# Performance work log

Hardware: AMD Instinct MI355X
Metric: run time of the kernel (lower is better)

The kernel has to match this reference:

```python
import jax, jax.numpy as jnp
import numpy as np

N = 4096          # batch size / number of points
D_DATA = 1024     # data feature dim
D_LATENT = 64     # latent dim
REG_LAMBDA = 0.5


def _pdist(x):
    """Pairwise Euclidean distance matrix [N, N] via the gram trick.

    Equivalent to norm(x[None, :, :] - x[:, None, :], axis=-1) but avoids the
    N x N x D intermediate. Safe sqrt so the (zero) diagonal has zero gradient.
    """
    sq = jnp.sum(x * x, axis=-1)                      # [N]
    g = x @ x.T                                       # [N, N] gram
    d2 = jnp.maximum(sq[:, None] + sq[None, :] - 2.0 * g, 0.0)
    pos = d2 > 0
    d = jnp.sqrt(jnp.where(pos, d2, 1.0))
    return jnp.where(pos, d, 0.0)


def _mst_edges(dist):
    """Edges (i, j) of the minimum spanning tree of the complete graph with
    edge weights dist[i, j] (0d persistent homology death edges).
    Prim's algorithm, vectorized per step via lax.scan. Returns [N-1, 2] int32.
    """
    n = dist.shape[0]
    in_tree = jnp.zeros(n, dtype=bool).at[0].set(True)
    min_dist = dist[0]                                # best distance to tree
    min_src = jnp.zeros(n, dtype=jnp.int32)           # tree node achieving it

    def step(carry, _):
        in_tree, min_dist, min_src = carry
        masked = jnp.where(in_tree, jnp.inf, min_dist)
        j = jnp.argmin(masked).astype(jnp.int32)
        edge = jnp.stack([min_src[j], j])
        in_tree = in_tree.at[j].set(True)
        dj = dist[j]
        upd = dj < min_dist
        min_dist = jnp.where(upd, dj, min_dist)
        min_src = jnp.where(upd, j, min_src)
        return (in_tree, min_dist, min_src), edge

    _, edges = jax.lax.scan(step, (in_tree, min_dist, min_src), None, length=n - 1)
    return edges  # [N-1, 2]


def _gather(dist, edges):
    return dist[edges[:, 0], edges[:, 1]]  # [N-1]


def setup_inputs() -> dict:
    key = jax.random.key(0)
    k1, k2, k3 = jax.random.split(key, 3)
    return {
        "y_true": jax.random.normal(k1, (N, D_DATA), dtype=jnp.float32),
        "latent": jax.random.normal(k2, (N, D_LATENT), dtype=jnp.float32),
        "y_pred": jax.random.normal(k3, (N, D_DATA), dtype=jnp.float32),
        "latent_norm": jnp.array(1.0, dtype=jnp.float32),
    }


def reference(y_true, latent, y_pred, latent_norm):
    # keras MSE: mean over last axis -> per-sample vector [N]
    ae_loss = jnp.mean((y_true - y_pred) ** 2, axis=-1)

    data_distances = _pdist(y_true)
    data_distances = data_distances / jnp.max(data_distances)
    latent_distances = _pdist(latent) / latent_norm

    e_data = _mst_edges(jax.lax.stop_gradient(data_distances))
    data_loss = jnp.mean((_gather(data_distances, e_data)
                          - _gather(latent_distances, e_data)) ** 2)

    e_lat = _mst_edges(jax.lax.stop_gradient(latent_distances))
    latent_loss = jnp.mean((_gather(data_distances, e_lat)
                            - _gather(latent_distances, e_lat)) ** 2)

    topo_loss = data_loss + latent_loss
    return ae_loss + REG_LAMBDA * topo_loss  # [N] (scalar topo broadcast)
```

## Files before the change

kernel.cpp:

```cpp
#include <hip/hip_runtime.h>
#include <math.h>

#define N_PTS 4096
#define DD 1024
#define DL 64
#define NEDGE (N_PTS - 1)
#define B_ROUNDS 12
#define NT 32

typedef __attribute__((ext_vector_type(8))) short short8;
typedef __attribute__((ext_vector_type(4))) float floatx4;
typedef __attribute__((ext_vector_type(4))) unsigned short ushortx4;

__device__ __forceinline__ unsigned short f2bf(float f) {
  unsigned u = __float_as_uint(f);
  u = u + 0x7FFFu + ((u >> 16) & 1u);
  return (unsigned short)(u >> 16);
}

__global__ __launch_bounds__(256) void ae_sq_kernel(const float* __restrict__ yt,
                                                    const float* __restrict__ yp,
                                                    float* __restrict__ out,
                                                    float* __restrict__ sqD,
                                                    unsigned short* __restrict__ Xb) {
  int row = blockIdx.x, tid = threadIdx.x;
  const float4* a = (const float4*)(yt + (size_t)row * DD);
  const float4* b = (const float4*)(yp + (size_t)row * DD);
  float4 va = a[tid], vb = b[tid];
  ushortx4 o = {f2bf(va.x), f2bf(va.y), f2bf(va.z), f2bf(va.w)};
  *(ushortx4*)(Xb + (size_t)row * DD + tid * 4) = o;
  float e0 = va.x - vb.x, e1 = va.y - vb.y, e2 = va.z - vb.z, e3 = va.w - vb.w;
  float se = e0 * e0 + e1 * e1 + e2 * e2 + e3 * e3;
  float ss = va.x * va.x + va.y * va.y + va.z * va.z + va.w * va.w;
  for (int off = 32; off > 0; off >>= 1) {
    se += __shfl_down(se, off);
    ss += __shfl_down(ss, off);
  }
  __shared__ float sse[4], sss[4];
  int lane = tid & 63, w = tid >> 6;
  if (lane == 0) { sse[w] = se; sss[w] = ss; }
  __syncthreads();
  if (tid == 0) {
    out[row] = (sse[0] + sse[1] + sse[2] + sse[3]) * (1.0f / DD);
    sqD[row] = sss[0] + sss[1] + sss[2] + sss[3];
  }
}

__global__ __launch_bounds__(256) void sql_kernel(const float* __restrict__ lat,
                                                  float* __restrict__ sqL,
                                                  unsigned short* __restrict__ Lb) {
  int row = blockIdx.x * 4 + (threadIdx.x >> 6);
  int lane = threadIdx.x & 63;
  float v = lat[(size_t)row * DL + lane];
  Lb[(size_t)row * DL + lane] = f2bf(v);
  float s = v * v;
  for (int off = 32; off > 0; off >>= 1) s += __shfl_down(s, off);
  if (lane == 0) sqL[row] = s;
}

__global__ __launch_bounds__(256) void boruvka_init(unsigned short* __restrict__ comp,
                                                    unsigned long long* __restrict__ bestKey,
                                                    int* __restrict__ numRoots,
                                                    int* __restrict__ edgeCnt,
                                                    const float* __restrict__ sqD,
                                                    const float* __restrict__ sqL,
                                                    unsigned int* __restrict__ normbits) {
  int i = blockIdx.x * 256 + threadIdx.x;
  if (i < N_PTS) {
    comp[i] = (unsigned short)i;
    comp[N_PTS + i] = (unsigned short)i;
    bestKey[i] = ~0ULL;
    bestKey[N_PTS + i] = ~0ULL;
  }
  if (i == 0) {
    numRoots[0] = N_PTS; numRoots[1] = N_PTS;
    edgeCnt[0] = 0; edgeCnt[1] = 0;
  }
  if (blockIdx.x < 2) {
    const float* s = blockIdx.x ? sqL : sqD;
    int tid = threadIdx.x;
    float m = 0.f;
#pragma unroll
    for (int k = 0; k < 16; ++k) m = fmaxf(m, s[tid + k * 256]);
    for (int off = 32; off > 0; off >>= 1) m = fmaxf(m, __shfl_down(m, off));
    __shared__ float sm[4];
    int lane = tid & 63, w = tid >> 6;
    if (lane == 0) sm[w] = m;
    __syncthreads();
    if (tid == 0)
      normbits[blockIdx.x] = __float_as_uint(fmaxf(fmaxf(sm[0], sm[1]), fmaxf(sm[2], sm[3])));
  }
}

__global__ __launch_bounds__(256) void dist_mfma(const unsigned short* __restrict__ Xb,
                                                 const unsigned short* __restrict__ Lb,
                                                 const float* __restrict__ sqD,
                                                 const float* __restrict__ sqL,
                                                 unsigned short* __restrict__ dD,
                                                 unsigned short* __restrict__ dL,
                                                 const unsigned int* __restrict__ normbits,
                                                 unsigned int* __restrict__ maxbits) {
  int inst = blockIdx.y;
  const unsigned short* X = inst ? Lb : Xb;
  const float* sq = inst ? sqL : sqD;
  unsigned short* dist = inst ? dL : dD;
  int K = inst ? DL : DD;
  float scale = 65535.0f / (2.0f * sqrtf(__uint_as_float(normbits[inst])) + 1e-12f);

  int bi = 0, rem = blockIdx.x, span = NT;
  while (rem >= span) { rem -= span; ++bi; --span; }
  int bj = bi + rem;
  int row0 = bi * 128, col0 = bj * 128;

  __shared__ short As[128 * 40];
  __shared__ short Bs[128 * 40];
  int tid = threadIdx.x;
  int wave = tid >> 6, lane = tid & 63;
  int m = lane & 15, q = lane >> 4;
  int rw = (wave >> 1) * 64, cw = (wave & 1) * 64;

  floatx4 acc[4][4];
#pragma unroll
  for (int mi = 0; mi < 4; ++mi)
#pragma unroll
    for (int ni = 0; ni < 4; ++ni) acc[mi][ni] = {0.f, 0.f, 0.f, 0.f};

  int s0 = tid, s1 = tid + 256;
  int r0 = s0 >> 2, p0 = s0 & 3, r1 = s1 >> 2, p1 = s1 & 3;

  for (int k0 = 0; k0 < K; k0 += 32) {
    short8 a0 = *(const short8*)(X + (size_t)(row0 + r0) * K + k0 + p0 * 8);
    short8 a1 = *(const short8*)(X + (size_t)(row0 + r1) * K + k0 + p1 * 8);
    short8 b0 = *(const short8*)(X + (size_t)(col0 + r0) * K + k0 + p0 * 8);
    short8 b1 = *(const short8*)(X + (size_t)(col0 + r1) * K + k0 + p1 * 8);
    __syncthreads();
    *(short8*)&As[r0 * 40 + p0 * 8] = a0;
    *(short8*)&As[r1 * 40 + p1 * 8] = a1;
    *(short8*)&Bs[r0 * 40 + p0 * 8] = b0;
    *(short8*)&Bs[r1 * 40 + p1 * 8] = b1;
    __syncthreads();
    short8 aF[4], bF[4];
#pragma unroll
    for (int mi = 0; mi < 4; ++mi)
      aF[mi] = *(const short8*)&As[(rw + mi * 16 + m) * 40 + q * 8];
#pragma unroll
    for (int ni = 0; ni < 4; ++ni)
      bF[ni] = *(const short8*)&Bs[(cw + ni * 16 + m) * 40 + q * 8];
#pragma unroll
    for (int mi = 0; mi < 4; ++mi)
#pragma unroll
      for (int ni = 0; ni < 4; ++ni)
        acc[mi][ni] = __builtin_amdgcn_mfma_f32_16x16x32_bf16(aF[mi], bF[ni],
                                                              acc[mi][ni], 0, 0, 0);
  }

  float bmax = 0.f;
#pragma unroll
  for (int mi = 0; mi < 4; ++mi) {
    int i0 = row0 + rw + mi * 16 + q * 4;
    float s_i[4] = {sq[i0], sq[i0 + 1], sq[i0 + 2], sq[i0 + 3]};
#pragma unroll
    for (int ni = 0; ni < 4; ++ni) {
      int j = col0 + cw + ni * 16 + m;
      float sj = sq[j];
      ushortx4 tvec;
#pragma unroll
      for (int r = 0; r < 4; ++r) {
        float d2 = s_i[r] + sj - 2.f * acc[mi][ni][r];
        float d = d2 > 0.f ? sqrtf(d2) : 0.f;
        bmax = fmaxf(bmax, d);
        unsigned short u = (unsigned short)fminf(d * scale, 65535.0f);
        dist[(size_t)(i0 + r) * N_PTS + j] = u;
        tvec[r] = u;
      }
      *(ushortx4*)&dist[(size_t)j * N_PTS + i0] = tvec;
    }
  }
  if (inst == 0) {
    for (int off = 32; off > 0; off >>= 1) bmax = fmaxf(bmax, __shfl_down(bmax, off));
    __shared__ float bm[4];
    if (lane == 0) bm[wave] = bmax;
    __syncthreads();
    if (tid == 0)
      atomicMax(maxbits, __float_as_uint(fmaxf(fmaxf(bm[0], bm[1]), fmaxf(bm[2], bm[3]))));
  }
}

__global__ __launch_bounds__(256) void boruvka_scan0(const unsigned short* __restrict__ dD,
                                                     const unsigned short* __restrict__ dL,
                                                     unsigned int* __restrict__ segKey,
                                                     unsigned long long* __restrict__ bestKey) {
  int inst = blockIdx.y;
  const unsigned short* dist = inst ? dL : dD;
  unsigned int* segK = segKey + (size_t)inst * N_PTS * 64;
  unsigned long long* bkI = bestKey + (size_t)inst * N_PTS;
  int tid = threadIdx.x, wave = tid >> 6, lane = tid & 63;
  int row = blockIdx.x * 4 + wave;
  const uint4* rowp = (const uint4*)(dist + (size_t)row * N_PTS);
  unsigned mk = 0xFFFFFFFFu, fk = 0xFFFFFFFFu;
  int colbase = lane * 64;
#pragma unroll
  for (int t = 0; t < 8; ++t) {
    uint4 v = rowp[lane * 8 + t];
    unsigned e[8] = {v.x & 0xFFFFu, v.x >> 16, v.y & 0xFFFFu, v.y >> 16,
                     v.z & 0xFFFFu, v.z >> 16, v.w & 0xFFFFu, v.w >> 16};
#pragma unroll
    for (int u = 0; u < 8; ++u) {
      int col = colbase + t * 8 + u;
      unsigned key = (e[u] << 12) | (unsigned)col;
      mk = min(mk, key);
      if (col != row) fk = min(fk, key);
    }
  }
  segK[(size_t)row * 64 + lane] = mk;
#pragma unroll
  for (int off = 32; off > 0; off >>= 1) fk = min(fk, __shfl_xor(fk, off));
  if (lane == 0) {
    unsigned dd16 = fk >> 12;
    int j = (int)(fk & 0xFFFu);
    int lo = row < j ? row : j, hi = row < j ? j : row;
    bkI[row] = ((unsigned long long)dd16 << 24) |
               ((unsigned long long)lo << 12) | (unsigned long long)hi;
  }
}

__global__ __launch_bounds__(256) void boruvka_scan(const unsigned short* __restrict__ dD,
                                                    const unsigned short* __restrict__ dL,
                                                    const unsigned int* __restrict__ segKey,
                                                    const unsigned short* __restrict__ comp,
                                                    unsigned long long* __restrict__ bestKey,
                                                    const int* __restrict__ numRoots) {
  int inst = blockIdx.y;
  if (numRoots[inst] <= 1) return;
  const unsigned short* dist = inst ? dL : dD;
  const unsigned int* segK = segKey + (size_t)inst * N_PTS * 64;
  const unsigned short* compI = comp + (size_t)inst * N_PTS;
  unsigned long long* bkI = bestKey + (size_t)inst * N_PTS;
  int tid = threadIdx.x, wave = tid >> 6, lane = tid & 63;

  int row = blockIdx.x * 4 + wave;
  unsigned myc = compI[row];
  unsigned skey = segK[(size_t)row * 64 + lane];
#pragma unroll
  for (int k = 2; k <= 64; k <<= 1)
#pragma unroll
    for (int j = k >> 1; j > 0; j >>= 1) {
      unsigned p = __shfl_xor(skey, j);
      unsigned mn = min(skey, p), mx = max(skey, p);
      skey = (((lane & k) == 0) == ((lane & j) == 0)) ? mn : mx;
    }
  unsigned best = 0xFFFFFFFFu;
  const unsigned short* rowp = dist + (size_t)row * N_PTS;
  int i = 0;
  while (i < 64) {
    unsigned k0 = __shfl(skey, i);
    if (k0 >= best) break;
    unsigned k1 = (i < 63) ? __shfl(skey, i + 1) : 0xFFFFFFFFu;
    int b0 = (int)(k0 & 0xFC0u);
    unsigned d0v = rowp[b0 + lane];
    unsigned c0v = compI[b0 + lane];
    unsigned cand = (c0v != myc) ? ((d0v << 12) | (unsigned)(b0 + lane)) : 0xFFFFFFFFu;
    if (k1 < best) {
      int b1 = (int)(k1 & 0xFC0u);
      unsigned d1v = rowp[b1 + lane];
      unsigned c1v = compI[b1 + lane];
      unsigned c2 = (c1v != myc) ? ((d1v << 12) | (unsigned)(b1 + lane)) : 0xFFFFFFFFu;
      cand = min(cand, c2);
    }
#pragma unroll
    for (int off = 32; off > 0; off >>= 1) cand = min(cand, __shfl_xor(cand, off));
    best = min(best, cand);
    i += 2;
  }
  if (lane == 0 && best != 0xFFFFFFFFu) {
    unsigned dd16 = best >> 12;
    int j = (int)(best & 0xFFFu);
    int lo = row < j ? row : j, hi = row < j ? j : row;
    unsigned long long key40 = ((unsigned long long)dd16 << 24) |
                               ((unsigned long long)lo << 12) | (unsigned long long)hi;
    if (key40 < bkI[myc]) atomicMin(&bkI[myc], key40);
  }
}

__global__ __launch_bounds__(1024) void boruvka_merge(unsigned short* __restrict__ comp,
                                                      unsigned long long* __restrict__ bestKey,
                                                      int* __restrict__ numRoots,
                                                      int2* __restrict__ edges,
                                                      int* __restrict__ edgeCnt) {
  int inst = blockIdx.x;
  if (numRoots[inst] <= 1) return;
  unsigned short* compI = comp + (size_t)inst * N_PTS;
  unsigned long long* bkI = bestKey + (size_t)inst * N_PTS;
  edges += (size_t)inst * NEDGE;

  __shared__ unsigned short comp_s[N_PTS];
  __shared__ unsigned short parent_s[N_PTS];
  __shared__ unsigned long long key_s[N_PTS];
  __shared__ int wtot[16], wbase[16];
  __shared__ int rootCnt, changed;
  int tid = threadIdx.x, lane = tid & 63, w = tid >> 6;
  if (tid == 0) rootCnt = 0;
  for (int i = tid; i < N_PTS / 8; i += 1024)
    ((uint4*)comp_s)[i] = ((const uint4*)compI)[i];
  for (int i = tid; i < N_PTS / 2; i += 1024)
    ((uint4*)key_s)[i] = ((const uint4*)bkI)[i];
  __syncthreads();

  int cnt = 0;
  int2 ebuf[4];
#pragma unroll
  for (int k = 0; k < 4; ++k) {
    int c = tid + k * 1024;
    unsigned short p = (unsigned short)c;
    if (comp_s[c] == c) {
      unsigned long long key = key_s[c];
      bkI[c] = ~0ULL;
      if (key != ~0ULL) {
        int lo = (int)((key >> 12) & 0xFFF), hi = (int)(key & 0xFFF);
        int c2 = (comp_s[lo] == c) ? comp_s[hi] : comp_s[lo];
        bool mutual = (key_s[c2] == key);
        bool add;
        if (mutual) {
          if (c < c2) add = true;
          else { p = (unsigned short)c2; add = false; }
        } else { p = (unsigned short)c2; add = true; }
        if (add) ebuf[cnt++] = make_int2(lo, hi);
      }
    }
    parent_s[c] = p;
  }
  int ws = cnt;
#pragma unroll
  for (int off = 1; off < 64; off <<= 1) {
    int v = __shfl_up(ws, off);
    if (lane >= off) ws += v;
  }
  if (lane == 63) wtot[w] = ws;
  __syncthreads();
  if (tid == 0) {
    int acc = edgeCnt[inst];
    for (int k = 0; k < 16; ++k) { wbase[k] = acc; acc += wtot[k]; }
    edgeCnt[inst] = acc;
  }
  __syncthreads();
  int base = wbase[w] + ws - cnt;
  for (int k = 0; k < cnt; ++k)
    if (base + k < NEDGE) edges[base + k] = ebuf[k];
  for (int it = 0; it < 12; ++it) {
    if (tid == 0) changed = 0;
    __syncthreads();
    int any = 0;
#pragma unroll
    for (int k = 0; k < 4; ++k) {
      int c = tid + k * 1024;
      unsigned short p = parent_s[c];
      unsigned short pp = parent_s[p];
      if (pp != p) { parent_s[c] = pp; any = 1; }
    }
    if (any) changed = 1;
    __syncthreads();
    if (!changed) break;
  }
  int local = 0;
#pragma unroll
  for (int k = 0; k < 4; ++k) {
    int c = tid + k * 1024;
    unsigned short old = comp_s[c];
    if (old == (unsigned short)c && parent_s[c] == (unsigned short)c) local++;
    compI[c] = parent_s[old];
  }
  for (int off = 32; off > 0; off >>= 1) local += __shfl_down(local, off);
  if (lane == 0) atomicAdd(&rootCnt, local);
  __syncthreads();
  if (tid == 0) numRoots[inst] = rootCnt;
}

__global__ __launch_bounds__(256) void loss_kernel(const unsigned short* __restrict__ dD,
                                                   const unsigned short* __restrict__ dL,
                                                   const int2* __restrict__ edges_all,
                                                   const unsigned int* __restrict__ maxbits,
                                                   const unsigned int* __restrict__ normbits,
                                                   const float* __restrict__ latent_norm,
                                                   float* __restrict__ sums) {
  int tid = threadIdx.x;
  int e = blockIdx.x * 256 + tid;
  float facD = (2.0f * sqrtf(__uint_as_float(normbits[0])) + 1e-12f) * (1.0f / 65535.0f) /
               __uint_as_float(*maxbits);
  float facL = (2.0f * sqrtf(__uint_as_float(normbits[1])) + 1e-12f) * (1.0f / 65535.0f) /
               latent_norm[0];
  float v0 = 0.f, v1 = 0.f;
  if (e < 2 * NEDGE) {
    int2 ed = edges_all[e];
    int i = ed.x & (N_PTS - 1), j = ed.y & (N_PTS - 1);
    float dd = (float)dD[(size_t)i * N_PTS + j] * facD;
    float ld = (float)dL[(size_t)i * N_PTS + j] * facL;
    float df = dd - ld;
    if (e < NEDGE) v0 = df * df; else v1 = df * df;
  }
  for (int off = 32; off > 0; off >>= 1) {
    v0 += __shfl_down(v0, off);
    v1 += __shfl_down(v1, off);
  }
  __shared__ float s0[4], s1[4];
  int lane = tid & 63, w = tid >> 6;
  if (lane == 0) { s0[w] = v0; s1[w] = v1; }
  __syncthreads();
  if (tid == 0) {
    float t0 = s0[0] + s0[1] + s0[2] + s0[3];
    float t1 = s1[0] + s1[1] + s1[2] + s1[3];
    if (t0 != 0.f) atomicAdd(&sums[0], t0);
    if (t1 != 0.f) atomicAdd(&sums[1], t1);
  }
}

__global__ __launch_bounds__(256) void finalize_kernel(float* __restrict__ out,
                                                       const float* __restrict__ sums) {
  int i = blockIdx.x * blockDim.x + threadIdx.x;
  float topo = (sums[0] + sums[1]) * (1.0f / NEDGE);
  out[i] += 0.5f * topo;
}

extern "C" void kernel_launch(void* const* d_in, const int* in_sizes, int n_in,
                              void* d_out, int out_size, void* d_ws, size_t ws_size,
                              hipStream_t stream) {
  const float* y_true = (const float*)d_in[0];
  const float* latent = (const float*)d_in[1];
  const float* y_pred = (const float*)d_in[2];
  const float* latent_norm = (const float*)d_in[3];
  float* out = (float*)d_out;
  char* ws = (char*)d_ws;

  const size_t MAT16 = (size_t)N_PTS * N_PTS * 2;
  size_t off = 0;
  unsigned short* dD = (unsigned short*)(ws + off); off += MAT16;
  unsigned short* dL = (unsigned short*)(ws + off); off += MAT16;
  unsigned short* Xb = (unsigned short*)(ws + off); off += (size_t)N_PTS * DD * 2;
  unsigned short* Lb = (unsigned short*)(ws + off); off += (size_t)N_PTS * DL * 2;
  float* sqD = (float*)(ws + off); off += (size_t)N_PTS * 4;
  float* sqL = (float*)(ws + off); off += (size_t)N_PTS * 4;
  int2* edges = (int2*)(ws + off); off += (size_t)2 * NEDGE * 8 + 16;
  unsigned long long* bestKey = (unsigned long long*)(ws + off); off += (size_t)2 * N_PTS * 8;
  unsigned short* comp = (unsigned short*)(ws + off); off += (size_t)2 * N_PTS * 2;
  unsigned int* segKey = (unsigned int*)(ws + off); off += (size_t)2 * N_PTS * 64 * 4;
  int* numRoots = (int*)(ws + off); off += 256;
  int* edgeCnt = numRoots + 2;
  unsigned int* maxbits = (unsigned int*)(edgeCnt + 2);
  float* sums = (float*)(maxbits + 1);
  unsigned int* normbits = (unsigned int*)(sums + 2);

  hipMemsetAsync(numRoots, 0, 256, stream);

  ae_sq_kernel<<<N_PTS, 256, 0, stream>>>(y_true, y_pred, out, sqD, Xb);
  sql_kernel<<<N_PTS / 4, 256, 0, stream>>>(latent, sqL, Lb);
  boruvka_init<<<N_PTS / 256, 256, 0, stream>>>(comp, bestKey, numRoots, edgeCnt,
                                                sqD, sqL, normbits);

  int tri = NT * (NT + 1) / 2;
  dist_mfma<<<dim3(tri, 2), 256, 0, stream>>>(Xb, Lb, sqD, sqL, dD, dL, normbits, maxbits);

  boruvka_scan0<<<dim3(N_PTS / 4, 2), 256, 0, stream>>>(dD, dL, segKey, bestKey);
  boruvka_merge<<<2, 1024, 0, stream>>>(comp, bestKey, numRoots, edges, edgeCnt);
  for (int r = 1; r < B_ROUNDS; ++r) {
    boruvka_scan<<<dim3(N_PTS / 4, 2), 256, 0, stream>>>(dD, dL, segKey, comp, bestKey,
                                                         numRoots);
    boruvka_merge<<<2, 1024, 0, stream>>>(comp, bestKey, numRoots, edges, edgeCnt);
  }

  loss_kernel<<<32, 256, 0, stream>>>(dD, dL, edges, maxbits, normbits, latent_norm, sums);
  finalize_kernel<<<N_PTS / 256, 256, 0, stream>>>(out, sums);
}
```

Measured before the change: 260.8 us.

## Fuse prep and loss kernels, drop memset, quantize squared distances

After: 271.7 us. +4.2%, slower.

```diff
diff --git a/kernel.cpp b/kernel.cpp
--- a/kernel.cpp
+++ b/kernel.cpp
@@ -18,44 +18,46 @@
   return (unsigned short)(u >> 16);
 }
 
-__global__ __launch_bounds__(256) void ae_sq_kernel(const float* __restrict__ yt,
-                                                    const float* __restrict__ yp,
-                                                    float* __restrict__ out,
-                                                    float* __restrict__ sqD,
-                                                    unsigned short* __restrict__ Xb) {
-  int row = blockIdx.x, tid = threadIdx.x;
-  const float4* a = (const float4*)(yt + (size_t)row * DD);
-  const float4* b = (const float4*)(yp + (size_t)row * DD);
-  float4 va = a[tid], vb = b[tid];
-  ushortx4 o = {f2bf(va.x), f2bf(va.y), f2bf(va.z), f2bf(va.w)};
-  *(ushortx4*)(Xb + (size_t)row * DD + tid * 4) = o;
-  float e0 = va.x - vb.x, e1 = va.y - vb.y, e2 = va.z - vb.z, e3 = va.w - vb.w;
-  float se = e0 * e0 + e1 * e1 + e2 * e2 + e3 * e3;
-  float ss = va.x * va.x + va.y * va.y + va.z * va.z + va.w * va.w;
-  for (int off = 32; off > 0; off >>= 1) {
-    se += __shfl_down(se, off);
-    ss += __shfl_down(ss, off);
-  }
-  __shared__ float sse[4], sss[4];
-  int lane = tid & 63, w = tid >> 6;
-  if (lane == 0) { sse[w] = se; sss[w] = ss; }
-  __syncthreads();
-  if (tid == 0) {
-    out[row] = (sse[0] + sse[1] + sse[2] + sse[3]) * (1.0f / DD);
-    sqD[row] = sss[0] + sss[1] + sss[2] + sss[3];
-  }
-}
-
-__global__ __launch_bounds__(256) void sql_kernel(const float* __restrict__ lat,
-                                                  float* __restrict__ sqL,
-                                                  unsigned short* __restrict__ Lb) {
-  int row = blockIdx.x * 4 + (threadIdx.x >> 6);
-  int lane = threadIdx.x & 63;
-  float v = lat[(size_t)row * DL + lane];
-  Lb[(size_t)row * DL + lane] = f2bf(v);
-  float s = v * v;
-  for (int off = 32; off > 0; off >>= 1) s += __shfl_down(s, off);
-  if (lane == 0) sqL[row] = s;
+__global__ __launch_bounds__(256) void ae_sql_kernel(const float* __restrict__ yt,
+                                                     const float* __restrict__ yp,
+                                                     const float* __restrict__ lat,
+                                                     float* __restrict__ out,
+                                                     float* __restrict__ sqD,
+                                                     float* __restrict__ sqL,
+                                                     unsigned short* __restrict__ Xb,
+                                                     unsigned short* __restrict__ Lb) {
+  int tid = threadIdx.x;
+  if (blockIdx.x < N_PTS) {
+    int row = blockIdx.x;
+    const float4* a = (const float4*)(yt + (size_t)row * DD);
+    const float4* b = (const float4*)(yp + (size_t)row * DD);
+    float4 va = a[tid], vb = b[tid];
+    ushortx4 o = {f2bf(va.x), f2bf(va.y), f2bf(va.z), f2bf(va.w)};
+    *(ushortx4*)(Xb + (size_t)row * DD + tid * 4) = o;
+    float e0 = va.x - vb.x, e1 = va.y - vb.y, e2 = va.z - vb.z, e3 = va.w - vb.w;
+    float se = e0 * e0 + e1 * e1 + e2 * e2 + e3 * e3;
+    float ss = va.x * va.x + va.y * va.y + va.z * va.z + va.w * va.w;
+    for (int off = 32; off > 0; off >>= 1) {
+      se += __shfl_down(se, off);
+      ss += __shfl_down(ss, off);
+    }
+    __shared__ float sse[4], sss[4];
+    int lane = tid & 63, w = tid >> 6;
+    if (lane == 0) { sse[w] = se; sss[w] = ss; }
+    __syncthreads();
+    if (tid == 0) {
+      out[row] = (sse[0] + sse[1] + sse[2] + sse[3]) * (1.0f / DD);
+      sqD[row] = sss[0] + sss[1] + sss[2] + sss[3];
+    }
+  } else {
+    int row = (blockIdx.x - N_PTS) * 4 + (tid >> 6);
+    int lane = tid & 63;
+    float v = lat[(size_t)row * DL + lane];
+    Lb[(size_t)row * DL + lane] = f2bf(v);
+    float s = v * v;
+    for (int off = 32; off > 0; off >>= 1) s += __shfl_down(s, off);
+    if (lane == 0) sqL[row] = s;
+  }
 }
 
 __global__ __launch_bounds__(256) void boruvka_init(unsigned short* __restrict__ comp,
@@ -64,7 +66,9 @@
                                                     int* __restrict__ edgeCnt,
                                                     const float* __restrict__ sqD,
                                                     const float* __restrict__ sqL,
-                                                    unsigned int* __restrict__ normbits) {
+                                                    unsigned int* __restrict__ normbits,
+                                                    unsigned int* __restrict__ maxbits,
+                                                    float* __restrict__ sums) {
   int i = blockIdx.x * 256 + threadIdx.x;
   if (i < N_PTS) {
     comp[i] = (unsigned short)i;
@@ -75,6 +79,8 @@
   if (i == 0) {
     numRoots[0] = N_PTS; numRoots[1] = N_PTS;
     edgeCnt[0] = 0; edgeCnt[1] = 0;
+    maxbits[0] = 0;
+    sums[0] = 0.f; sums[1] = 0.f;
   }
   if (blockIdx.x < 2) {
     const float* s = blockIdx.x ? sqL : sqD;
@@ -105,7 +111,7 @@
   const float* sq = inst ? sqL : sqD;
   unsigned short* dist = inst ? dL : dD;
   int K = inst ? DL : DD;
-  float scale = 65535.0f / (2.0f * sqrtf(__uint_as_float(normbits[inst])) + 1e-12f);
+  float scale2 = 65535.0f / (4.0f * __uint_as_float(normbits[inst]) + 1e-12f);
 
   int bi = 0, rem = blockIdx.x, span = NT;
   while (rem >= span) { rem -= span; ++bi; --span; }
@@ -167,9 +173,9 @@
 #pragma unroll
       for (int r = 0; r < 4; ++r) {
         float d2 = s_i[r] + sj - 2.f * acc[mi][ni][r];
-        float d = d2 > 0.f ? sqrtf(d2) : 0.f;
-        bmax = fmaxf(bmax, d);
-        unsigned short u = (unsigned short)fminf(d * scale, 65535.0f);
+        d2 = d2 > 0.f ? d2 : 0.f;
+        bmax = fmaxf(bmax, d2);
+        unsigned short u = (unsigned short)fminf(d2 * scale2, 65535.0f);
         dist[(size_t)(i0 + r) * N_PTS + j] = u;
         tvec[r] = u;
       }
@@ -375,49 +381,47 @@
   if (tid == 0) numRoots[inst] = rootCnt;
 }
 
-__global__ __launch_bounds__(256) void loss_kernel(const unsigned short* __restrict__ dD,
-                                                   const unsigned short* __restrict__ dL,
-                                                   const int2* __restrict__ edges_all,
-                                                   const unsigned int* __restrict__ maxbits,
-                                                   const unsigned int* __restrict__ normbits,
-                                                   const float* __restrict__ latent_norm,
-                                                   float* __restrict__ sums) {
-  int tid = threadIdx.x;
-  int e = blockIdx.x * 256 + tid;
-  float facD = (2.0f * sqrtf(__uint_as_float(normbits[0])) + 1e-12f) * (1.0f / 65535.0f) /
-               __uint_as_float(*maxbits);
-  float facL = (2.0f * sqrtf(__uint_as_float(normbits[1])) + 1e-12f) * (1.0f / 65535.0f) /
-               latent_norm[0];
+__global__ __launch_bounds__(1024) void loss_final_kernel(const unsigned short* __restrict__ dD,
+                                                          const unsigned short* __restrict__ dL,
+                                                          const int2* __restrict__ edges_all,
+                                                          const unsigned int* __restrict__ maxbits,
+                                                          const unsigned int* __restrict__ normbits,
+                                                          const float* __restrict__ latent_norm,
+                                                          float* __restrict__ out) {
+  int tid = threadIdx.x, lane = tid & 63, w = tid >> 6;
+  float fac2D = (4.0f * __uint_as_float(normbits[0]) + 1e-12f) * (1.0f / 65535.0f);
+  float fac2L = (4.0f * __uint_as_float(normbits[1]) + 1e-12f) * (1.0f / 65535.0f);
+  float inv_md = 1.0f / sqrtf(__uint_as_float(*maxbits));
+  float inv_ln = 1.0f / latent_norm[0];
   float v0 = 0.f, v1 = 0.f;
-  if (e < 2 * NEDGE) {
+#pragma unroll
+  for (int k = 0; k < 8; ++k) {
+    int e = tid + k * 1024;
+    if (e >= 2 * NEDGE) break;
     int2 ed = edges_all[e];
     int i = ed.x & (N_PTS - 1), j = ed.y & (N_PTS - 1);
-    float dd = (float)dD[(size_t)i * N_PTS + j] * facD;
-    float ld = (float)dL[(size_t)i * N_PTS + j] * facL;
+    float dd = sqrtf((float)dD[(size_t)i * N_PTS + j] * fac2D) * inv_md;
+    float ld = sqrtf((float)dL[(size_t)i * N_PTS + j] * fac2L) * inv_ln;
     float df = dd - ld;
-    if (e < NEDGE) v0 = df * df; else v1 = df * df;
+    if (e < NEDGE) v0 += df * df; else v1 += df * df;
   }
   for (int off = 32; off > 0; off >>= 1) {
     v0 += __shfl_down(v0, off);
     v1 += __shfl_down(v1, off);
   }
-  __shared__ float s0[4], s1[4];
-  int lane = tid & 63, w = tid >> 6;
+  __shared__ float s0[16], s1[16];
+  __shared__ float topo_s;
   if (lane == 0) { s0[w] = v0; s1[w] = v1; }
   __syncthreads();
   if (tid == 0) {
-    float t0 = s0[0] + s0[1] + s0[2] + s0[3];
-    float t1 = s1[0] + s1[1] + s1[2] + s1[3];
-    if (t0 != 0.f) atomicAdd(&sums[0], t0);
-    if (t1 != 0.f) atomicAdd(&sums[1], t1);
-  }
-}
-
-__global__ __launch_bounds__(256) void finalize_kernel(float* __restrict__ out,
-                                                       const float* __restrict__ sums) {
-  int i = blockIdx.x * blockDim.x + threadIdx.x;
-  float topo = (sums[0] + sums[1]) * (1.0f / NEDGE);
-  out[i] += 0.5f * topo;
+    float t0 = 0.f, t1 = 0.f;
+    for (int k = 0; k < 16; ++k) { t0 += s0[k]; t1 += s1[k]; }
+    topo_s = 0.5f * (t0 + t1) * (1.0f / NEDGE);
+  }
+  __syncthreads();
+  float add = topo_s;
+#pragma unroll
+  for (int k = 0; k < 4; ++k) out[tid + k * 1024] += add;
 }
 
 extern "C" void kernel_launch(void* const* d_in, const int* in_sizes, int n_in,
@@ -448,12 +452,10 @@
   float* sums = (float*)(maxbits + 1);
   unsigned int* normbits = (unsigned int*)(sums + 2);
 
-  hipMemsetAsync(numRoots, 0, 256, stream);
-
-  ae_sq_kernel<<<N_PTS, 256, 0, stream>>>(y_true, y_pred, out, sqD, Xb);
-  sql_kernel<<<N_PTS / 4, 256, 0, stream>>>(latent, sqL, Lb);
+  ae_sql_kernel<<<N_PTS + N_PTS / 4, 256, 0, stream>>>(y_true, y_pred, latent, out,
+                                                       sqD, sqL, Xb, Lb);
   boruvka_init<<<N_PTS / 256, 256, 0, stream>>>(comp, bestKey, numRoots, edgeCnt,
-                                                sqD, sqL, normbits);
+                                                sqD, sqL, normbits, maxbits, sums);
 
   int tri = NT * (NT + 1) / 2;
   dist_mfma<<<dim3(tri, 2), 256, 0, stream>>>(Xb, Lb, sqD, sqL, dD, dL, normbits, maxbits);
@@ -466,6 +468,6 @@
     boruvka_merge<<<2, 1024, 0, stream>>>(comp, bestKey, numRoots, edges, edgeCnt);
   }
 
-  loss_kernel<<<32, 256, 0, stream>>>(dD, dL, edges, maxbits, normbits, latent_norm, sums);
-  finalize_kernel<<<N_PTS / 256, 256, 0, stream>>>(out, sums);
-}
+  loss_final_kernel<<<1, 1024, 0, stream>>>(dD, dL, edges, maxbits, normbits,
+                                            latent_norm, out);
+}
```
